# Kernel optimization log

Hardware: AMD Instinct MI355X
Metric: run time of the kernel (lower is better)

Reference implementation:

```python
import jax, jax.numpy as jnp
import numpy as np

N = 100000
E = 1600000
D = 64        # HID_NODE_ENC == HID_EDGE_ENC
H = 128       # HIDDEN_NODE_ONE
EPS = 1e-5
NEG_SLOPE = 0.01


def _xavier(key, shape):
    fan_in, fan_out = shape[0], shape[1]
    limit = float(np.sqrt(6.0 / (fan_in + fan_out)))
    return jax.random.uniform(key, shape, jnp.float32, -limit, limit)


def setup_inputs() -> dict:
    key = jax.random.key(0)
    ks = jax.random.split(key, 10)
    x = jax.random.normal(ks[0], (N, D), jnp.float32)
    edge_index = jax.random.randint(ks[1], (2, E), 0, N, jnp.int64)
    edge_attr = jax.random.normal(ks[2], (E, D), jnp.float32)
    u = jax.random.normal(ks[3], (1, 16), jnp.float32)
    batch = jnp.zeros((N,), jnp.int64)
    b_init = jnp.float32(0.01)
    params = {
        # node_mlp_1: Lin(128->128), LeakyReLU, BN(128), Lin(128->128)
        "W1": _xavier(ks[4], (2 * D, H)), "b1": jnp.full((H,), b_init),
        "g1": jnp.ones((H,), jnp.float32), "be1": jnp.zeros((H,), jnp.float32),
        "W2": _xavier(ks[5], (H, H)), "b2": jnp.full((H,), b_init),
        # node_mlp_2: Lin(192->128), LeakyReLU, BN(128), Lin(128->64)
        "W3": _xavier(ks[6], (H + D, H)), "b3": jnp.full((H,), b_init),
        "g2": jnp.ones((H,), jnp.float32), "be2": jnp.zeros((H,), jnp.float32),
        "W4": _xavier(ks[7], (H, D)), "b4": jnp.full((D,), b_init),
    }
    return {"x": x, "edge_index": edge_index, "edge_attr": edge_attr,
            "u": u, "batch": batch, **params}


def _bn(h, gamma, beta):
    # BatchNorm1d in training mode: biased batch statistics
    mean = jnp.mean(h, axis=0)
    var = jnp.mean(jnp.square(h - mean), axis=0)
    return (h - mean) * jax.lax.rsqrt(var + EPS) * gamma + beta


def reference(x, edge_index, edge_attr, u, batch,
              W1, b1, g1, be1, W2, b2,
              W3, b3, g2, be2, W4, b4):
    row, col = edge_index[0], edge_index[1]
    # gather + concat: [E, 2D]
    h = jnp.concatenate([x[row], edge_attr], axis=1)
    # node_mlp_1
    h = jax.nn.leaky_relu(h @ W1 + b1, NEG_SLOPE)
    h = _bn(h, g1, be1)
    h = h @ W2 + b2                       # [E, H]
    # scatter_add by destination node
    agg = jax.ops.segment_sum(h, col, num_segments=x.shape[0])  # [N, H]
    # concat with node feats, node_mlp_2
    h2 = jnp.concatenate([x, agg], axis=1)  # [N, H+D]
    h2 = jax.nn.leaky_relu(h2 @ W3 + b3, NEG_SLOPE)
    h2 = _bn(h2, g2, be2)
    return h2 @ W4 + b4                    # [N, D]
```

## Files before the change

### kernel.cpp

```cpp
#include <hip/hip_runtime.h>

#define NN 100000
#define NE 1600000
#define NTILE_E (NE / 128)
#define NTILE_N 782

typedef __attribute__((ext_vector_type(4))) float f32x4;
typedef __attribute__((ext_vector_type(8))) short s16x8;

__device__ __forceinline__ unsigned short f2bf(float f) {
  unsigned u = __builtin_bit_cast(unsigned, f);
  u = (u + 0x7FFFu + ((u >> 16) & 1u)) >> 16;
  return (unsigned short)u;
}
__device__ __forceinline__ void pack4(float4 v, unsigned short* dst) {
  ushort4 h;
  h.x = f2bf(v.x); h.y = f2bf(v.y); h.z = f2bf(v.z); h.w = f2bf(v.w);
  *(ushort4*)dst = h;
}

__global__ void k0_prep(const float* __restrict__ W1, const float* __restrict__ W3,
                        unsigned short* __restrict__ W1bT, unsigned short* __restrict__ W3bT) {
  int i = blockIdx.x * 256 + threadIdx.x;
  if (i < 16384) {
    int n = i >> 7, k = i & 127;
    W1bT[i] = f2bf(W1[k * 128 + n]);
  } else if (i < 16384 + 24576) {
    int j = i - 16384;
    int n = j / 192, k = j % 192;
    W3bT[j] = f2bf(W3[k * 128 + n]);
  }
}

__global__ void k_hist(const int* __restrict__ eidx, int* __restrict__ hist) {
  int e = blockIdx.x * 256 + threadIdx.x;
  if (e < NE) atomicAdd(&hist[eidx[NE + e]], 1);
}

__global__ void k_scan(int* __restrict__ hist, float* __restrict__ cntF) {
  __shared__ int ssum[1024];
  const int t = threadIdx.x;
  const int base = t * 98;
  const int cl = (base >= NN) ? 0 : ((NN - base < 98) ? (NN - base) : 98);
  int s = 0;
  for (int i = 0; i < cl; i++) s += hist[base + i];
  ssum[t] = s;
  __syncthreads();
  for (int d = 1; d < 1024; d <<= 1) {
    int v = (t >= d) ? ssum[t - d] : 0;
    __syncthreads();
    ssum[t] += v;
    __syncthreads();
  }
  int run = (t == 0) ? 0 : ssum[t - 1];
  for (int i = 0; i < cl; i++) {
    int hv = hist[base + i];
    hist[base + i] = run;
    cntF[base + i] = (float)hv;
    run += hv;
  }
}

__global__ void k_scatter(const int* __restrict__ eidx, int* __restrict__ off,
                          int2* __restrict__ pairS) {
  int e = blockIdx.x * 256 + threadIdx.x;
  if (e < NE) {
    int c = eidx[NE + e];
    int p = atomicAdd(&off[c], 1);
    pairS[p] = make_int2(c, e);
  }
}

__global__ __attribute__((amdgpu_flat_work_group_size(512, 512)))
__attribute__((amdgpu_waves_per_eu(4))) void k1_edge(
    const float* __restrict__ x, const int* __restrict__ eidx,
    const float* __restrict__ ea, const unsigned short* __restrict__ W1bT,
    const float* __restrict__ b1, const int2* __restrict__ pairS,
    float* __restrict__ S, float* __restrict__ stat1) {
  __shared__ __align__(16) char HAt[67584];
  __shared__ int rIdx2[2][128];
  __shared__ int eIdx2[2][128];
  __shared__ int colT2[2][132];
  __shared__ float sred[256];
  unsigned short (*At)[136] = (unsigned short (*)[136])HAt;
  float (*H)[132] = (float (*)[132])HAt;

  const int tid = threadIdx.x;
  const int wave = tid >> 6, lane = tid & 63;
  const int l15 = lane & 15, quad = lane >> 4;
  const int rowbase = (wave >> 2) * 64;
  const int colbase = (wave & 3) * 32;

  s16x8 bfrag[2][4];
#pragma unroll
  for (int ct = 0; ct < 2; ct++)
#pragma unroll
    for (int ks = 0; ks < 4; ks++)
      bfrag[ct][ks] = *(const s16x8*)(W1bT + (colbase + ct * 16 + l15) * 128 + ks * 32 + quad * 8);

  float b1j[2];
#pragma unroll
  for (int ct = 0; ct < 2; ct++) b1j[ct] = b1[colbase + ct * 16 + l15];

  float lsum[2] = {0, 0}, lsq[2] = {0, 0};

  {
    const int eb = blockIdx.x * 128;
    if (tid < 128) {
      int2 pr = pairS[eb + tid];
      eIdx2[0][tid] = pr.y;
      rIdx2[0][tid] = eidx[pr.y];
      colT2[0][tid + 1] = pr.x;
    } else if (tid == 128) {
      colT2[0][0] = (eb > 0) ? pairS[eb - 1].x : -1;
    } else if (tid == 129) {
      colT2[0][129] = (eb + 128 < NE) ? pairS[eb + 128].x : -1;
    }
  }

  int p = 0;
  for (int tile = blockIdx.x; tile < NTILE_E; tile += gridDim.x) {
    __syncthreads();
#pragma unroll
    for (int i = 0; i < 4; i++) {
      int idx = tid + i * 512; int e = idx >> 4, c = idx & 15;
      float4 v = ((const float4*)x)[(size_t)rIdx2[p][e] * 16 + c];
      pack4(v, &At[e][c * 4]);
    }
#pragma unroll
    for (int i = 0; i < 4; i++) {
      int idx = tid + i * 512; int e = idx >> 4, c = idx & 15;
      float4 v = ((const float4*)ea)[(size_t)eIdx2[p][e] * 16 + c];
      pack4(v, &At[e][64 + c * 4]);
    }
    {
      const int ntile = tile + gridDim.x;
      if (ntile < NTILE_E) {
        const int eb2 = ntile * 128;
        if (tid < 128) {
          int2 pr = pairS[eb2 + tid];
          eIdx2[p ^ 1][tid] = pr.y;
          rIdx2[p ^ 1][tid] = eidx[pr.y];
          colT2[p ^ 1][tid + 1] = pr.x;
        } else if (tid == 128) {
          colT2[p ^ 1][0] = pairS[eb2 - 1].x;
        } else if (tid == 129) {
          colT2[p ^ 1][129] = (eb2 + 128 < NE) ? pairS[eb2 + 128].x : -1;
        }
      }
    }
    __syncthreads();

    f32x4 acc[4][2];
#pragma unroll
    for (int rt = 0; rt < 4; rt++)
#pragma unroll
      for (int ct = 0; ct < 2; ct++) acc[rt][ct] = (f32x4){0.f, 0.f, 0.f, 0.f};

#pragma unroll
    for (int ks = 0; ks < 4; ks++) {
      s16x8 af[4];
#pragma unroll
      for (int rt = 0; rt < 4; rt++)
        af[rt] = *(const s16x8*)&At[rowbase + rt * 16 + l15][ks * 32 + quad * 8];
#pragma unroll
      for (int rt = 0; rt < 4; rt++)
#pragma unroll
        for (int ct = 0; ct < 2; ct++)
          acc[rt][ct] = __builtin_amdgcn_mfma_f32_16x16x32_bf16(af[rt], bfrag[ct][ks], acc[rt][ct], 0, 0, 0);
    }

    __syncthreads();
#pragma unroll
    for (int rt = 0; rt < 4; rt++)
#pragma unroll
      for (int r = 0; r < 4; r++) {
        const int er = rowbase + rt * 16 + quad * 4 + r;
#pragma unroll
        for (int ct = 0; ct < 2; ct++) {
          float v = acc[rt][ct][r] + b1j[ct];
          v = v > 0.0f ? v : 0.01f * v;
          lsum[ct] += v; lsq[ct] += v * v;
          H[er][colbase + ct * 16 + l15] = v;
        }
      }
    __syncthreads();

    {
      const int col = tid & 127;
      const int r0 = (tid >> 7) * 32;
      float runsum = H[r0][col];
      int runstart = r0;
      int curnode = colT2[p][r0 + 1];
      for (int r = r0 + 1; r < r0 + 32; ++r) {
        int nd = colT2[p][r + 1];
        float v = H[r][col];
        if (nd == curnode) { runsum += v; }
        else {
          float* pp = S + (size_t)curnode * 128 + col;
          if (colT2[p][runstart] != curnode) *pp = runsum;
          else atomicAdd(pp, runsum);
          curnode = nd; runsum = v; runstart = r;
        }
      }
      float* pp = S + (size_t)curnode * 128 + col;
      if (colT2[p][runstart] != curnode && colT2[p][r0 + 33] != curnode) *pp = runsum;
      else atomicAdd(pp, runsum);
    }
    p ^= 1;
  }

  if (tid < 256) sred[tid] = 0.0f;
  __syncthreads();
#pragma unroll
  for (int ct = 0; ct < 2; ct++) {
    float s = lsum[ct], q = lsq[ct];
    s += __shfl_down(s, 32); q += __shfl_down(q, 32);
    s += __shfl_down(s, 16); q += __shfl_down(q, 16);
    if (lane < 16) {
      atomicAdd(&sred[colbase + ct * 16 + l15], s);
      atomicAdd(&sred[128 + colbase + ct * 16 + l15], q);
    }
  }
  __syncthreads();
  if (tid < 256) atomicAdd(&stat1[tid], sred[tid]);
}

__global__ void k2_fold1(const float* __restrict__ stat1, const float* __restrict__ g1,
                         const float* __restrict__ be1, const float* __restrict__ W2,
                         const float* __restrict__ b2,
                         unsigned short* __restrict__ W2pT, float* __restrict__ v128) {
  __shared__ float s1s[128], t1s[128];
  __shared__ float red[256];
  const int tid = threadIdx.x;
  if (tid < 128) {
    float mean = stat1[tid] * (1.0f / NE);
    float var = stat1[128 + tid] * (1.0f / NE) - mean * mean;
    float rstd = rsqrtf(var + 1e-5f);
    float s = g1[tid] * rstd;
    s1s[tid] = s; t1s[tid] = be1[tid] - mean * s;
  }
  __syncthreads();
  const int b = blockIdx.x;
  if (b < 16) {
#pragma unroll
    for (int j = 0; j < 4; j++) {
      int i = b * 1024 + j * 256 + tid;
      int k = i >> 7, n = i & 127;
      W2pT[n * 128 + k] = f2bf(s1s[k] * W2[i]);
    }
  } else {
    int j = tid & 127, hh = tid >> 7;
    float p = 0.f;
    for (int k = hh * 64; k < hh * 64 + 64; k++) p += t1s[k] * W2[k * 128 + j];
    red[tid] = p;
    __syncthreads();
    if (tid < 128) v128[tid] = red[tid] + red[tid + 128] + b2[tid];
  }
}

__global__ __launch_bounds__(256, 2) void k3_node(
    const float* __restrict__ x, const float* __restrict__ S, const float* __restrict__ cnt,
    const unsigned short* __restrict__ W2pT, const float* __restrict__ v128,
    const unsigned short* __restrict__ W3bT, const float* __restrict__ b3,
    unsigned short* __restrict__ tOut, float* __restrict__ stat2) {
  __shared__ unsigned short Abuf[128][136];
  __shared__ unsigned short Xbuf[128][72];
  __shared__ float cbuf[128];
  __shared__ float sred[256];

  const int tid = threadIdx.x;
  const int wave = tid >> 6, lane = tid & 63;
  const int l15 = lane & 15, quad = lane >> 4;
  const int rowbase = (wave >> 1) * 64;
  const int colbase = (wave & 1) * 64;

  float vj[4], b3j[4];
#pragma unroll
  for (int ct = 0; ct < 4; ct++) {
    int jc = colbase + ct * 16 + l15;
    vj[ct] = v128[jc]; b3j[ct] = b3[jc];
  }
  float lsum[4] = {0, 0, 0, 0}, lsq[4] = {0, 0, 0, 0};

  for (int t = blockIdx.x; t < NTILE_N; t += gridDim.x) {
    const int nb = t * 128;
    __syncthreads();
#pragma unroll
    for (int i = 0; i < 16; i++) {
      int idx = tid + i * 256; int e = idx >> 5, c = idx & 31;
      int node = nb + e;
      float4 v = {0.f, 0.f, 0.f, 0.f};
      if (node < NN) v = ((const float4*)S)[(size_t)node * 32 + c];
      pack4(v, &Abuf[e][c * 4]);
    }
#pragma unroll
    for (int i = 0; i < 8; i++) {
      int idx = tid + i * 256; int e = idx >> 4, c = idx & 15;
      int node = nb + e;
      float4 v = {0.f, 0.f, 0.f, 0.f};
      if (node < NN) v = ((const float4*)x)[(size_t)node * 16 + c];
      pack4(v, &Xbuf[e][c * 4]);
    }
    if (tid < 128) cbuf[tid] = (nb + tid < NN) ? cnt[nb + tid] : 0.0f;
    __syncthreads();

    f32x4 acc[4][4];
#pragma unroll
    for (int rt = 0; rt < 4; rt++)
#pragma unroll
      for (int ct = 0; ct < 4; ct++) acc[rt][ct] = (f32x4){0.f, 0.f, 0.f, 0.f};
#pragma unroll
    for (int ks = 0; ks < 4; ks++) {
      s16x8 af[4];
#pragma unroll
      for (int rt = 0; rt < 4; rt++)
        af[rt] = *(const s16x8*)&Abuf[rowbase + rt * 16 + l15][ks * 32 + quad * 8];
      s16x8 bfr[4];
#pragma unroll
      for (int ct = 0; ct < 4; ct++)
        bfr[ct] = *(const s16x8*)(W2pT + (colbase + ct * 16 + l15) * 128 + ks * 32 + quad * 8);
#pragma unroll
      for (int rt = 0; rt < 4; rt++)
#pragma unroll
        for (int ct = 0; ct < 4; ct++)
          acc[rt][ct] = __builtin_amdgcn_mfma_f32_16x16x32_bf16(af[rt], bfr[ct], acc[rt][ct], 0, 0, 0);
    }
    __syncthreads();
#pragma unroll
    for (int rt = 0; rt < 4; rt++)
#pragma unroll
      for (int r = 0; r < 4; r++) {
        int er = rowbase + rt * 16 + quad * 4 + r;
#pragma unroll
        for (int ct = 0; ct < 4; ct++) {
          float val = acc[rt][ct][r] + cbuf[er] * vj[ct];
          Abuf[er][colbase + ct * 16 + l15] = f2bf(val);
        }
      }
    __syncthreads();

    f32x4 acc2[4][4];
#pragma unroll
    for (int rt = 0; rt < 4; rt++)
#pragma unroll
      for (int ct = 0; ct < 4; ct++) acc2[rt][ct] = (f32x4){0.f, 0.f, 0.f, 0.f};
#pragma unroll
    for (int ks = 0; ks < 6; ks++) {
      s16x8 af[4];
      if (ks < 2) {
#pragma unroll
        for (int rt = 0; rt < 4; rt++)
          af[rt] = *(const s16x8*)&Xbuf[rowbase + rt * 16 + l15][ks * 32 + quad * 8];
      } else {
#pragma unroll
        for (int rt = 0; rt < 4; rt++)
          af[rt] = *(const s16x8*)&Abuf[rowbase + rt * 16 + l15][(ks - 2) * 32 + quad * 8];
      }
      s16x8 bfr[4];
#pragma unroll
      for (int ct = 0; ct < 4; ct++)
        bfr[ct] = *(const s16x8*)(W3bT + (size_t)(colbase + ct * 16 + l15) * 192 + ks * 32 + quad * 8);
#pragma unroll
      for (int rt = 0; rt < 4; rt++)
#pragma unroll
        for (int ct = 0; ct < 4; ct++)
          acc2[rt][ct] = __builtin_amdgcn_mfma_f32_16x16x32_bf16(af[rt], bfr[ct], acc2[rt][ct], 0, 0, 0);
    }

#pragma unroll
    for (int rt = 0; rt < 4; rt++)
#pragma unroll
      for (int r = 0; r < 4; r++) {
        int er = rowbase + rt * 16 + quad * 4 + r;
        int node = nb + er;
        if (node < NN) {
#pragma unroll
          for (int ct = 0; ct < 4; ct++) {
            float val = acc2[rt][ct][r] + b3j[ct];
            val = val > 0.0f ? val : 0.01f * val;
            lsum[ct] += val; lsq[ct] += val * val;
            tOut[(size_t)node * 128 + colbase + ct * 16 + l15] = f2bf(val);
          }
        }
      }
  }

  sred[tid] = 0.0f;
  __syncthreads();
#pragma unroll
  for (int ct = 0; ct < 4; ct++) {
    float s = lsum[ct], q = lsq[ct];
    s += __shfl_down(s, 32); q += __shfl_down(q, 32);
    s += __shfl_down(s, 16); q += __shfl_down(q, 16);
    if (lane < 16) {
      atomicAdd(&sred[colbase + ct * 16 + l15], s);
      atomicAdd(&sred[128 + colbase + ct * 16 + l15], q);
    }
  }
  __syncthreads();
  atomicAdd(&stat2[tid], sred[tid]);
}

__global__ void k5_fold2(const float* __restrict__ stat2, const float* __restrict__ g2,
                         const float* __restrict__ be2, const float* __restrict__ W4,
                         const float* __restrict__ b4,
                         unsigned short* __restrict__ W4fT, float* __restrict__ b4f) {
  __shared__ float s2s[128], t2s[128];
  __shared__ float red[256];
  const int tid = threadIdx.x;
  if (tid < 128) {
    float mean = stat2[tid] * (1.0f / NN);
    float var = stat2[128 + tid] * (1.0f / NN) - mean * mean;
    float rstd = rsqrtf(var + 1e-5f);
    float s = g2[tid] * rstd;
    s2s[tid] = s; t2s[tid] = be2[tid] - mean * s;
  }
  __syncthreads();
  const int b = blockIdx.x;
  if (b < 8) {
#pragma unroll
    for (int j = 0; j < 4; j++) {
      int i = b * 1024 + j * 256 + tid;
      int k = i >> 6, n = i & 63;
      W4fT[n * 128 + k] = f2bf(s2s[k] * W4[i]);
    }
  } else {
    int j = tid & 63, part = tid >> 6;
    float p = 0.f;
    for (int k = part * 32; k < part * 32 + 32; k++) p += t2s[k] * W4[k * 64 + j];
    red[tid] = p;
    __syncthreads();
    if (tid < 64) b4f[tid] = red[tid] + red[tid + 64] + red[tid + 128] + red[tid + 192] + b4[tid];
  }
}

__global__ __launch_bounds__(256, 2) void k6_out(
    const unsigned short* __restrict__ tIn, const unsigned short* __restrict__ W4fT,
    const float* __restrict__ b4f, float* __restrict__ out) {
  __shared__ unsigned short Abuf[128][136];
  const int tid = threadIdx.x;
  const int wave = tid >> 6, lane = tid & 63;
  const int l15 = lane & 15, quad = lane >> 4;
  const int rowbase = (wave >> 1) * 64;
  const int colbase = (wave & 1) * 32;

  s16x8 bfrag[2][4];
#pragma unroll
  for (int ct = 0; ct < 2; ct++)
#pragma unroll
    for (int ks = 0; ks < 4; ks++)
      bfrag[ct][ks] = *(const s16x8*)(W4fT + (colbase + ct * 16 + l15) * 128 + ks * 32 + quad * 8);
  float bj[2];
#pragma unroll
  for (int ct = 0; ct < 2; ct++) bj[ct] = b4f[colbase + ct * 16 + l15];

  for (int t = blockIdx.x; t < NTILE_N; t += gridDim.x) {
    const int nb = t * 128;
    __syncthreads();
#pragma unroll
    for (int i = 0; i < 8; i++) {
      int idx = tid + i * 256; int e = idx >> 4, c = idx & 15;
      int node = nb + e;
      s16x8 v = {0, 0, 0, 0, 0, 0, 0, 0};
      if (node < NN) v = *(const s16x8*)(tIn + (size_t)node * 128 + c * 8);
      *(s16x8*)&Abuf[e][c * 8] = v;
    }
    __syncthreads();

    f32x4 acc[4][2];
#pragma unroll
    for (int rt = 0; rt < 4; rt++)
#pragma unroll
      for (int ct = 0; ct < 2; ct++) acc[rt][ct] = (f32x4){0.f, 0.f, 0.f, 0.f};
#pragma unroll
    for (int ks = 0; ks < 4; ks++) {
      s16x8 af[4];
#pragma unroll
      for (int rt = 0; rt < 4; rt++)
        af[rt] = *(const s16x8*)&Abuf[rowbase + rt * 16 + l15][ks * 32 + quad * 8];
#pragma unroll
      for (int rt = 0; rt < 4; rt++)
#pragma unroll
        for (int ct = 0; ct < 2; ct++)
          acc[rt][ct] = __builtin_amdgcn_mfma_f32_16x16x32_bf16(af[rt], bfrag[ct][ks], acc[rt][ct], 0, 0, 0);
    }
#pragma unroll
    for (int rt = 0; rt < 4; rt++)
#pragma unroll
      for (int r = 0; r < 4; r++) {
        int er = rowbase + rt * 16 + quad * 4 + r;
        int node = nb + er;
        if (node < NN) {
#pragma unroll
          for (int ct = 0; ct < 2; ct++)
            out[(size_t)node * 64 + colbase + ct * 16 + l15] = acc[rt][ct][r] + bj[ct];
        }
      }
  }
}

extern "C" void kernel_launch(void* const* d_in, const int* in_sizes, int n_in,
                              void* d_out, int out_size, void* d_ws, size_t ws_size,
                              hipStream_t stream) {
  (void)in_sizes; (void)n_in; (void)out_size; (void)ws_size;
  const float* x   = (const float*)d_in[0];
  const int*   ei  = (const int*)d_in[1];
  const float* ea  = (const float*)d_in[2];
  const float* W1  = (const float*)d_in[5];
  const float* b1  = (const float*)d_in[6];
  const float* g1  = (const float*)d_in[7];
  const float* be1 = (const float*)d_in[8];
  const float* W2  = (const float*)d_in[9];
  const float* b2  = (const float*)d_in[10];
  const float* W3  = (const float*)d_in[11];
  const float* b3  = (const float*)d_in[12];
  const float* g2  = (const float*)d_in[13];
  const float* be2 = (const float*)d_in[14];
  const float* W4  = (const float*)d_in[15];
  const float* b4  = (const float*)d_in[16];
  float* out = (float*)d_out;

  char* w = (char*)d_ws;
  float* S     = (float*)(w);
  float* stat1 = (float*)(w + 51200000);
  float* stat2 = (float*)(w + 51201024);
  int*   hist  = (int*)  (w + 51202048);
  float* cntF  = (float*)(w + 51602432);
  unsigned short* W1bT = (unsigned short*)(w + 52002816);
  unsigned short* W3bT = (unsigned short*)(w + 52035584);
  unsigned short* W2pT = (unsigned short*)(w + 52084736);
  float* v128  = (float*)(w + 52117504);
  unsigned short* W4fT = (unsigned short*)(w + 52118016);
  float* b4f   = (float*)(w + 52134400);
  unsigned short* tOut = (unsigned short*)(w + 52134656);
  int2* pairS = (int2*)(w + 52134656);

  hipMemsetAsync(d_ws, 0, 51602432, stream);

  k0_prep<<<160, 256, 0, stream>>>(W1, W3, W1bT, W3bT);
  k_hist<<<6250, 256, 0, stream>>>(ei, hist);
  k_scan<<<1, 1024, 0, stream>>>(hist, cntF);
  k_scatter<<<6250, 256, 0, stream>>>(ei, hist, pairS);
  k1_edge<<<512, 512, 0, stream>>>(x, ei, ea, W1bT, b1, pairS, S, stat1);
  k2_fold1<<<17, 256, 0, stream>>>(stat1, g1, be1, W2, b2, W2pT, v128);
  k3_node<<<512, 256, 0, stream>>>(x, S, cntF, W2pT, v128, W3bT, b3, tOut, stat2);
  k5_fold2<<<9, 256, 0, stream>>>(stat2, g2, be2, W4, b4, W4fT, b4f);
  k6_out<<<512, 256, 0, stream>>>(tOut, W4fT, b4f, out);
}
```

Measured before the change: 1.209 ms.

## Prefetch next tile's gathered x/edge_attr rows into registers during segmented scatter

Gathers of x[row] and edge_attr for the next edge tile are now issued into registers (sx/se) right after the H write, so their global-memory latency overlaps the segmented scatter-add phase and the next loop iteration's barrier. The loop top uses a raw s_barrier with an lgkmcnt wait instead of __syncthreads so outstanding vector-memory loads are not forced to complete at the barrier. This costs 32 extra VGPRs per thread, which may reduce occupancy, and relies on the index arrays for the next tile being visible after the existing barrier.

Measured after the change: 1.295 ms. 7.1% more time.

```diff
diff --git a/kernel.cpp b/kernel.cpp
--- a/kernel.cpp
+++ b/kernel.cpp
@@ -117,37 +117,49 @@
       colT2[0][129] = (eb + 128 < NE) ? pairS[eb + 128].x : -1;
     }
   }
+  __syncthreads();
+
+  float4 sx[4], se[4];
+#pragma unroll
+  for (int i = 0; i < 4; i++) {
+    int idx = tid + i * 512; int e = idx >> 4, c = idx & 15;
+    sx[i] = ((const float4*)x)[(size_t)rIdx2[0][e] * 16 + c];
+  }
+#pragma unroll
+  for (int i = 0; i < 4; i++) {
+    int idx = tid + i * 512; int e = idx >> 4, c = idx & 15;
+    se[i] = ((const float4*)ea)[(size_t)eIdx2[0][e] * 16 + c];
+  }
 
   int p = 0;
   for (int tile = blockIdx.x; tile < NTILE_E; tile += gridDim.x) {
-    __syncthreads();
+    asm volatile("s_waitcnt lgkmcnt(0)" ::: "memory");
+    __builtin_amdgcn_s_barrier();
+    __builtin_amdgcn_sched_barrier(0);
+
+    const int ntile = tile + gridDim.x;
+    if (ntile < NTILE_E) {
+      const int eb2 = ntile * 128;
+      if (tid < 128) {
+        int2 pr = pairS[eb2 + tid];
+        eIdx2[p ^ 1][tid] = pr.y;
+        rIdx2[p ^ 1][tid] = eidx[pr.y];
+        colT2[p ^ 1][tid + 1] = pr.x;
+      } else if (tid == 128) {
+        colT2[p ^ 1][0] = pairS[eb2 - 1].x;
+      } else if (tid == 129) {
+        colT2[p ^ 1][129] = (eb2 + 128 < NE) ? pairS[eb2 + 128].x : -1;
+      }
+    }
 #pragma unroll
     for (int i = 0; i < 4; i++) {
       int idx = tid + i * 512; int e = idx >> 4, c = idx & 15;
-      float4 v = ((const float4*)x)[(size_t)rIdx2[p][e] * 16 + c];
-      pack4(v, &At[e][c * 4]);
+      pack4(sx[i], &At[e][c * 4]);
     }
 #pragma unroll
     for (int i = 0; i < 4; i++) {
       int idx = tid + i * 512; int e = idx >> 4, c = idx & 15;
-      float4 v = ((const float4*)ea)[(size_t)eIdx2[p][e] * 16 + c];
-      pack4(v, &At[e][64 + c * 4]);
-    }
-    {
-      const int ntile = tile + gridDim.x;
-      if (ntile < NTILE_E) {
-        const int eb2 = ntile * 128;
-        if (tid < 128) {
-          int2 pr = pairS[eb2 + tid];
-          eIdx2[p ^ 1][tid] = pr.y;
-          rIdx2[p ^ 1][tid] = eidx[pr.y];
-          colT2[p ^ 1][tid + 1] = pr.x;
-        } else if (tid == 128) {
-          colT2[p ^ 1][0] = pairS[eb2 - 1].x;
-        } else if (tid == 129) {
-          colT2[p ^ 1][129] = (eb2 + 128 < NE) ? pairS[eb2 + 128].x : -1;
-        }
-      }
+      pack4(se[i], &At[e][64 + c * 4]);
     }
     __syncthreads();
 
@@ -185,6 +197,19 @@
         }
       }
     __syncthreads();
+
+    if (ntile < NTILE_E) {
+#pragma unroll
+      for (int i = 0; i < 4; i++) {
+        int idx = tid + i * 512; int e = idx >> 4, c = idx & 15;
+        sx[i] = ((const float4*)x)[(size_t)rIdx2[p ^ 1][e] * 16 + c];
+      }
+#pragma unroll
+      for (int i = 0; i < 4; i++) {
+        int idx = tid + i * 512; int e = idx >> 4, c = idx & 15;
+        se[i] = ((const float4*)ea)[(size_t)eIdx2[p ^ 1][e] * 16 + c];
+      }
+    }
 
     {
       const int col = tid & 127;
```
